# Kernel tuning notes

Hardware: AMD Instinct MI355X
Metric: run time of the kernel (lower is better)

Reference implementation:

```python
import jax, jax.numpy as jnp
import numpy as np

N, D, K = 4096, 1024, 32
MARGIN = 0.3
OP_TYPE = "weighty"


def setup_inputs() -> dict:
    key = jax.random.key(0)
    k1, k2, k3, k4, k5 = jax.random.split(key, 5)
    return {
        "inputs": jax.random.normal(k1, (N, D), jnp.float32),
        "prediction": jax.random.normal(k2, (N, K), jnp.float32),
        "targets": jax.random.randint(k3, (N,), 0, K),
        "true_targets": jax.random.randint(k4, (N,), 0, K),
        "prob": jax.random.uniform(k5, (N,), jnp.float32),
        "threshold": jnp.float32(0.5),
    }


def _weighty(d1, d2, pair_type, op_type):
    # vectorized translation of weighty_new
    if op_type == "mean":
        return (d1 + d2) / 2.0
    if op_type == "max":
        return jnp.maximum(d1, d2)
    if op_type == "min":
        return jnp.minimum(d1, d2)
    if op_type == "max-min":
        return jnp.maximum(d1, d2) if pair_type == 1 else jnp.minimum(d1, d2)
    # op_type == 'weighty'
    if pair_type == 1:
        e1, e2 = jnp.exp(d1), jnp.exp(d2)
        return (e1 * d1 + e2 * d2) / (e1 + e2)
    e1, e2 = jnp.exp(-d1), jnp.exp(-d2)
    return (e1 * d1 + e2 * d2) / (e1 + e2 + 1e-6)


def reference(inputs, prediction, targets, true_targets, prob, threshold):
    n = inputs.shape[0]
    rows = jnp.arange(n)
    # pairwise euclidean dist (GEMM-based, matches addmm_ formulation)
    sq = jnp.sum(inputs * inputs, axis=1)
    dist = sq[:, None] + sq[None, :] - 2.0 * (inputs @ inputs.T)
    dist = jnp.sqrt(jnp.clip(dist, 1e-12, None))  # [n, n]

    same = targets[:, None] == targets[None, :]
    conf = prob >= threshold

    # negatives sorted ascending by dist; positives sorted descending by dist
    neg_order = jnp.argsort(jnp.where(~same, dist, jnp.inf), axis=1)   # [n,n]
    pos_order = jnp.argsort(jnp.where(same, -dist, jnp.inf), axis=1)   # [n,n]
    hp = pos_order[:, 0]   # hardest positive (max dist)
    hn = neg_order[:, 0]   # hardest negative (min dist)
    d_ap = dist[rows, hp]
    d_an = dist[rows, hn]

    cp = prob[hp] >= threshold
    cn = prob[hn] >= threshold
    fn = jnp.argmax(prediction, axis=1)[hn] == targets  # hard neg is a false negative

    # neg re-selection: ranks 1..10 first with prob>=t, else rank 11 (loop_cnt cap 10)
    neg_cand = neg_order[:, 1:12]                       # [n,11]
    ok_n = prob[neg_cand] >= threshold
    sel_n = jnp.where(ok_n[:, :10].any(axis=1), jnp.argmax(ok_n[:, :10], axis=1), 10)
    d_nn = dist[rows, neg_cand[rows, sel_n]]

    # pos re-selection: descending ranks 1..5 first with prob>=t, else rank 6 (loop_cnt cap 5)
    pos_cand = pos_order[:, 1:7]                        # [n,6]
    ok_p = prob[pos_cand] >= threshold
    sel_p = jnp.where(ok_p[:, :5].any(axis=1), jnp.argmax(ok_p[:, :5], axis=1), 5)
    d_np = dist[rows, pos_cand[rows, sel_p]]

    w1 = _weighty(d_ap, d_an, 1, OP_TYPE)
    w0 = _weighty(d_ap, d_an, 0, OP_TYPE)

    case_b = cp & (~cn) & fn                 # confident pos, unconfident FN neg
    case_cd = (~cp) & (cn | (~fn))           # unconfident pos branches that re-select pos
    inv = (~cp) & (~cn) & fn                 # inverse loss branch

    ap = jnp.where(case_b, w1, jnp.where(case_cd, d_np, d_ap))
    an = jnp.where(case_b, d_nn, jnp.where(case_cd, w0, d_an))

    per = jnp.where(inv,
                    jax.nn.relu(an - ap + MARGIN),
                    jax.nn.relu(ap - an + MARGIN))
    conff = conf.astype(per.dtype)
    cnt = jnp.sum(conf.astype(jnp.int32))
    loss = jnp.where(cnt > 0, jnp.sum(per * conff) / jnp.maximum(cnt, 1).astype(per.dtype), 0.0)
    correct = jnp.sum(((an >= ap) & conf).astype(jnp.int32))
    return loss, correct, cnt
```

## Files before the change

kernel.cpp:

```cpp
#include <hip/hip_runtime.h>
#include <hip/hip_bf16.h>
#include <stdint.h>

typedef _Float16 half8 __attribute__((ext_vector_type(8)));
typedef _Float16 half4 __attribute__((ext_vector_type(4)));
typedef float f32x4 __attribute__((ext_vector_type(4)));
typedef unsigned long long u64;

#define N_ROWS 4096
#define DIM 1024
#define KCLS 32
#define MARGIN_F 0.3f
#define SENTN 0xFFFFFFFFFFFFFFFFull

typedef const __attribute__((address_space(1))) void GASV;
typedef __attribute__((address_space(3))) void LASV;

__device__ __forceinline__ void gload_lds16(const void* g, void* l) {
    __builtin_amdgcn_global_load_lds((GASV*)g, (LASV*)l, 16, 0, 0);
}

__global__ __launch_bounds__(256) void prep_kernel(
    const float* __restrict__ inputs, const float* __restrict__ prediction,
    _Float16* __restrict__ xh, float* __restrict__ sq, int* __restrict__ pred_cls)
{
    int wid = threadIdx.x >> 6, lane = threadIdx.x & 63;
    int r = blockIdx.x * 4 + wid;
    const float* row = inputs + (size_t)r * DIM;
    _Float16* hrow = xh + (size_t)r * DIM;
    float s = 0.f;
#pragma unroll
    for (int c = 0; c < 4; ++c) {
        int idx = lane * 4 + c * 256;
        float4 v = *(const float4*)(row + idx);
        s += v.x * v.x + v.y * v.y + v.z * v.z + v.w * v.w;
        half4 h;
        h.x = (_Float16)v.x; h.y = (_Float16)v.y;
        h.z = (_Float16)v.z; h.w = (_Float16)v.w;
        *(half4*)(hrow + idx) = h;
    }
#pragma unroll
    for (int off = 32; off; off >>= 1) s += __shfl_xor(s, off);

    u64 key = 0ull;
    if (lane < KCLS) {
        unsigned b = __float_as_uint(prediction[(size_t)r * KCLS + lane]);
        unsigned u = (b & 0x80000000u) ? ~b : (b | 0x80000000u);
        key = ((u64)u << 32) | (unsigned)(KCLS - 1 - lane);
    }
#pragma unroll
    for (int off = 32; off; off >>= 1) {
        u64 o = __shfl_xor(key, off);
        if (o > key) key = o;
    }
    if (lane == 0) {
        sq[r] = s;
        pred_cls[r] = KCLS - 1 - (int)(key & 0xFFFFFFFFu);
    }
}

__global__ __launch_bounds__(512) void gemm_kernel(
    const _Float16* __restrict__ X, const float* __restrict__ sq,
    float* __restrict__ out, int mode, int rb0)
{
    __shared__ __align__(16) _Float16 As[128 * 64];
    __shared__ __align__(16) _Float16 Bs[128 * 64];
    int tid = threadIdx.x;

    int bx, by;
    bool diag = false, mirror = false;
    if (mode == 0) {
        int u = ((int)blockIdx.x & 7) * 66 + ((int)blockIdx.x >> 3);
        int t_ = (int)((sqrtf(8.f * u + 1.f) - 1.f) * 0.5f);
        while ((t_ + 1) * (t_ + 2) / 2 <= u) ++t_;
        while (t_ * (t_ + 1) / 2 > u) --t_;
        by = t_;
        bx = u - t_ * (t_ + 1) / 2;
        diag = (bx == by);
        mirror = !diag;
    } else {
        int nwg = gridDim.x;
        int q = nwg >> 3;
        int swz = ((int)blockIdx.x & 7) * q + ((int)blockIdx.x >> 3);
        int nbx = nwg / 32;
        bx = swz % nbx;
        by = swz / nbx;
    }

    int rs = tid >> 3;
    int ss = tid & 7;
    int srcslot = ss ^ (rs & 7);
    const _Float16* gA = X + (size_t)(rb0 + bx * 128 + rs) * DIM + srcslot * 8;
    const _Float16* gB = X + (size_t)(by * 128 + rs) * DIM + srcslot * 8;
    _Float16* lA = As + tid * 8;
    _Float16* lB = Bs + tid * 8;

    int wid = tid >> 6, lane = tid & 63;
    int wr = (wid >> 2) * 64, wc = (wid & 3) * 32;
    int fr = lane & 15, q4 = lane >> 4;

    f32x4 acc[4][2];
#pragma unroll
    for (int m = 0; m < 4; ++m)
#pragma unroll
        for (int n = 0; n < 2; ++n) acc[m][n] = (f32x4){0.f, 0.f, 0.f, 0.f};

    for (int k0 = 0; k0 < DIM; k0 += 64) {
#pragma unroll
        for (int p = 0; p < 2; ++p) {
            gload_lds16(gA + k0 + (size_t)(p * 64) * DIM, lA + p * 4096);
            if (!diag) gload_lds16(gB + k0 + (size_t)(p * 64) * DIM, lB + p * 4096);
        }
        __syncthreads();
        const _Float16* Bsrc = diag ? As : Bs;
#pragma unroll
        for (int ks = 0; ks < 2; ++ks) {
            half8 a[4], b[2];
#pragma unroll
            for (int m = 0; m < 4; ++m) {
                int row = wr + m * 16 + fr;
                int s = (ks * 4 + q4) ^ (row & 7);
                a[m] = *(const half8*)(As + row * 64 + s * 8);
            }
#pragma unroll
            for (int n = 0; n < 2; ++n) {
                int brow = wc + n * 16 + fr;
                int s = (ks * 4 + q4) ^ (brow & 7);
                b[n] = *(const half8*)(Bsrc + brow * 64 + s * 8);
            }
#pragma unroll
            for (int m = 0; m < 4; ++m)
#pragma unroll
                for (int n = 0; n < 2; ++n)
                    acc[m][n] = __builtin_amdgcn_mfma_f32_16x16x32_f16(a[m], b[n], acc[m][n], 0, 0, 0);
        }
        __syncthreads();
    }

    int rbase = rb0 + bx * 128 + wr + q4 * 4;
    float sqr_[4][4];
#pragma unroll
    for (int m = 0; m < 4; ++m)
#pragma unroll
        for (int q = 0; q < 4; ++q) sqr_[m][q] = sq[rbase + m * 16 + q];

#pragma unroll
    for (int n = 0; n < 2; ++n) {
        int col = by * 128 + wc + n * 16 + fr;
        float sqc = sq[col];
#pragma unroll
        for (int m = 0; m < 4; ++m) {
            int row0 = rbase + m * 16;
            float4 d;
            d.x = fmaxf(sqr_[m][0] + sqc - 2.f * acc[m][n][0], 1e-12f);
            d.y = fmaxf(sqr_[m][1] + sqc - 2.f * acc[m][n][1], 1e-12f);
            d.z = fmaxf(sqr_[m][2] + sqc - 2.f * acc[m][n][2], 1e-12f);
            d.w = fmaxf(sqr_[m][3] + sqc - 2.f * acc[m][n][3], 1e-12f);
            out[(size_t)(row0 + 0) * N_ROWS + col] = d.x;
            out[(size_t)(row0 + 1) * N_ROWS + col] = d.y;
            out[(size_t)(row0 + 2) * N_ROWS + col] = d.z;
            out[(size_t)(row0 + 3) * N_ROWS + col] = d.w;
            if (mirror)
                *(float4*)&out[(size_t)col * N_ROWS + row0] = d;
        }
    }
}

__global__ __launch_bounds__(256) void select_kernel(
    const float* __restrict__ dot,
    const int* __restrict__ targets, const float* __restrict__ prob,
    const int* __restrict__ pred_cls, const float* __restrict__ thr_p,
    int rb0, float* __restrict__ per_term, int* __restrict__ corr_flag)
{
    __shared__ u64 Tn[4], Tp[4];
    __shared__ u64 negCand[64];
    __shared__ u64 posCand[64];
    __shared__ unsigned cnts[2];
    __shared__ u64 sN[12], sP[7];
    __shared__ u64 red[4];
    __shared__ u64 bcast;

    int t = threadIdx.x, lane = t & 63, w = t >> 6;
    int rloc = blockIdx.x, r = rb0 + rloc;
    int tr = targets[r];
    const float* drow = dot + (size_t)rloc * N_ROWS;

    if (t < 64) { negCand[t] = SENTN; posCand[t] = 0ull; }
    if (t < 2) cnts[t] = 0u;

    unsigned bits[16];
    unsigned maskSame = 0;
    u64 mneg = SENTN, mpos = 0ull;
#pragma unroll
    for (int q = 0; q < 4; ++q) {
        int col0 = q * 1024 + t * 4;
        float4 dv = *(const float4*)(drow + col0);
        int4 tv = *(const int4*)(targets + col0);
        int j = q * 4;
        unsigned b;
        b = __float_as_uint(dv.x); bits[j + 0] = b;
        if (tv.x == tr) { maskSame |= 1u << (j + 0);
            u64 pk = ((u64)b << 32) | (unsigned)(N_ROWS - 1 - (col0 + 0)); mpos = pk > mpos ? pk : mpos;
        } else { u64 nk = ((u64)b << 32) | (unsigned)(col0 + 0); mneg = nk < mneg ? nk : mneg; }
        b = __float_as_uint(dv.y); bits[j + 1] = b;
        if (tv.y == tr) { maskSame |= 1u << (j + 1);
            u64 pk = ((u64)b << 32) | (unsigned)(N_ROWS - 1 - (col0 + 1)); mpos = pk > mpos ? pk : mpos;
        } else { u64 nk = ((u64)b << 32) | (unsigned)(col0 + 1); mneg = nk < mneg ? nk : mneg; }
        b = __float_as_uint(dv.z); bits[j + 2] = b;
        if (tv.z == tr) { maskSame |= 1u << (j + 2);
            u64 pk = ((u64)b << 32) | (unsigned)(N_ROWS - 1 - (col0 + 2)); mpos = pk > mpos ? pk : mpos;
        } else { u64 nk = ((u64)b << 32) | (unsigned)(col0 + 2); mneg = nk < mneg ? nk : mneg; }
        b = __float_as_uint(dv.w); bits[j + 3] = b;
        if (tv.w == tr) { maskSame |= 1u << (j + 3);
            u64 pk = ((u64)b << 32) | (unsigned)(N_ROWS - 1 - (col0 + 3)); mpos = pk > mpos ? pk : mpos;
        } else { u64 nk = ((u64)b << 32) | (unsigned)(col0 + 3); mneg = nk < mneg ? nk : mneg; }
    }

    u64 T3 = SENTN, m = mneg;
#pragma unroll
    for (int rd = 0; rd < 3; ++rd) {
        u64 b = m;
#pragma unroll
        for (int off = 32; off; off >>= 1) {
            u64 o = __shfl_xor(b, off);
            b = o < b ? o : b;
        }
        T3 = b;
        if (m == b) m = SENTN;
    }
    u64 P2 = 0ull, mp = mpos;
#pragma unroll
    for (int rd = 0; rd < 2; ++rd) {
        u64 b = mp;
#pragma unroll
        for (int off = 32; off; off >>= 1) {
            u64 o = __shfl_xor(b, off);
            b = o > b ? o : b;
        }
        P2 = b;
        if (mp == b) mp = 0ull;
    }
    if (lane == 0) { Tn[w] = T3; Tp[w] = P2; }
    __syncthreads();

    u64 Tneg = Tn[0];
    Tneg = Tn[1] > Tneg ? Tn[1] : Tneg;
    Tneg = Tn[2] > Tneg ? Tn[2] : Tneg;
    Tneg = Tn[3] > Tneg ? Tn[3] : Tneg;
    u64 Tpos = Tp[0];
    Tpos = Tp[1] < Tpos ? Tp[1] : Tpos;
    Tpos = Tp[2] < Tpos ? Tp[2] : Tpos;
    Tpos = Tp[3] < Tpos ? Tp[3] : Tpos;
    unsigned TnB = (unsigned)(Tneg >> 32);
    unsigned TpB = (unsigned)(Tpos >> 32);

#pragma unroll
    for (int q = 0; q < 4; ++q) {
#pragma unroll
        for (int e = 0; e < 4; ++e) {
            int j = q * 4 + e;
            int col = q * 1024 + t * 4 + e;
            unsigned b = bits[j];
            bool same = (maskSame >> j) & 1u;
            if (!same && b <= TnB) {
                unsigned s = atomicAdd(&cnts[0], 1u);
                if (s < 64u) negCand[s] = ((u64)b << 32) | (unsigned)col;
            }
            if (same && b >= TpB) {
                unsigned s = atomicAdd(&cnts[1], 1u);
                if (s < 64u) posCand[s] = ((u64)b << 32) | (unsigned)(N_ROWS - 1 - col);
            }
        }
    }
    __syncthreads();

    bool fb = (cnts[0] > 64u) || (cnts[1] > 64u);

    if (!fb) {
        if (w == 0) {
            u64 v = negCand[lane];
#pragma unroll
            for (int k = 2; k <= 64; k <<= 1) {
#pragma unroll
                for (int j = 32; j; j >>= 1) {
                    if (j >= k) continue;
                    u64 o = __shfl_xor(v, j);
                    bool up = (lane & k) == 0;
                    bool small = (lane & j) == 0;
                    bool keepmin = (small == up);
                    u64 lo = v < o ? v : o, hi = v < o ? o : v;
                    v = keepmin ? lo : hi;
                }
            }
            if (lane < 12) sN[lane] = v;
        } else if (w == 1) {
            u64 v = ~posCand[lane];
#pragma unroll
            for (int k = 2; k <= 64; k <<= 1) {
#pragma unroll
                for (int j = 32; j; j >>= 1) {
                    if (j >= k) continue;
                    u64 o = __shfl_xor(v, j);
                    bool up = (lane & k) == 0;
                    bool small = (lane & j) == 0;
                    bool keepmin = (small == up);
                    u64 lo = v < o ? v : o, hi = v < o ? o : v;
                    v = keepmin ? lo : hi;
                }
            }
            if (lane < 7) sP[lane] = ~v;
        }
    } else {
        unsigned remN = 0, remP = 0;
        for (int rd = 0; rd < 12; ++rd) {
            u64 best = SENTN;
#pragma unroll
            for (int q = 0; q < 4; ++q)
#pragma unroll
                for (int e = 0; e < 4; ++e) {
                    int j = q * 4 + e;
                    int col = q * 1024 + t * 4 + e;
                    bool valid = !((maskSame >> j) & 1u) && !((remN >> j) & 1u);
                    u64 nk = valid ? (((u64)bits[j] << 32) | (unsigned)col) : SENTN;
                    best = nk < best ? nk : best;
                }
#pragma unroll
            for (int off = 32; off; off >>= 1) {
                u64 o = __shfl_xor(best, off);
                best = o < best ? o : best;
            }
            if (lane == 0) red[w] = best;
            __syncthreads();
            if (t == 0) {
                u64 b0 = red[0];
                b0 = red[1] < b0 ? red[1] : b0;
                b0 = red[2] < b0 ? red[2] : b0;
                b0 = red[3] < b0 ? red[3] : b0;
                sN[rd] = b0; bcast = b0;
            }
            __syncthreads();
            u64 b0 = bcast;
#pragma unroll
            for (int q = 0; q < 4; ++q)
#pragma unroll
                for (int e = 0; e < 4; ++e) {
                    int j = q * 4 + e;
                    int col = q * 1024 + t * 4 + e;
                    if ((((u64)bits[j] << 32) | (unsigned)col) == b0) remN |= 1u << j;
                }
            __syncthreads();
        }
        for (int rd = 0; rd < 7; ++rd) {
            u64 best = 0ull;
#pragma unroll
            for (int q = 0; q < 4; ++q)
#pragma unroll
                for (int e = 0; e < 4; ++e) {
                    int j = q * 4 + e;
                    int col = q * 1024 + t * 4 + e;
                    bool valid = ((maskSame >> j) & 1u) && !((remP >> j) & 1u);
                    u64 pk = valid ? (((u64)bits[j] << 32) | (unsigned)(N_ROWS - 1 - col)) : 0ull;
                    best = pk > best ? pk : best;
                }
#pragma unroll
            for (int off = 32; off; off >>= 1) {
                u64 o = __shfl_xor(best, off);
                best = o > best ? o : best;
            }
            if (lane == 0) red[w] = best;
            __syncthreads();
            if (t == 0) {
                u64 b0 = red[0];
                b0 = red[1] > b0 ? red[1] : b0;
                b0 = red[2] > b0 ? red[2] : b0;
                b0 = red[3] > b0 ? red[3] : b0;
                sP[rd] = b0; bcast = b0;
            }
            __syncthreads();
            u64 b0 = bcast;
#pragma unroll
            for (int q = 0; q < 4; ++q)
#pragma unroll
                for (int e = 0; e < 4; ++e) {
                    int j = q * 4 + e;
                    int col = q * 1024 + t * 4 + e;
                    if ((((u64)bits[j] << 32) | (unsigned)(N_ROWS - 1 - col)) == b0) remP |= 1u << j;
                }
            __syncthreads();
        }
    }
    __syncthreads();

    if (w == 0) {
        float thr = *thr_p;
        u64 kN = (lane < 12) ? sN[lane] : SENTN;
        u64 kP = (lane >= 32 && lane < 39) ? sP[lane - 32] : 0ull;
        int idxN = ((int)(kN & 0xFFFFFFFFull)) & (N_ROWS - 1);
        int idxP = (N_ROWS - 1 - (int)(kP & 0xFFFFFFFFull)) & (N_ROWS - 1);
        bool confN = (lane < 12) && kN != SENTN && (prob[idxN] >= thr);
        bool confP = (lane >= 32 && lane < 39) && kP != 0ull && (prob[idxP] >= thr);
        u64 balN = __ballot(confN);
        u64 balP = __ballot(confP);

        u64 mN_ = balN & 0x7FEull;
        int selN = mN_ ? (__ffsll(mN_) - 1) : 11;
        unsigned dnn_bits = __shfl((unsigned)(kN >> 32), selN);
        u64 mP_ = balP & (0x3Eull << 32);
        int selP = mP_ ? (__ffsll(mP_) - 1) : 38;
        unsigned dnp_bits = __shfl((unsigned)(kP >> 32), selP);
        unsigned dap_bits = __shfl((unsigned)(kP >> 32), 32);

        if (lane == 0) {
            float d_ap = sqrtf(__uint_as_float(dap_bits));
            float d_an = sqrtf(__uint_as_float((unsigned)(kN >> 32)));
            int hn = idxN;
            bool cp = (balP >> 32) & 1ull;
            bool cn = balN & 1ull;
            bool fn = (pred_cls[hn] == tr);
            float d_nn = sqrtf(__uint_as_float(dnn_bits));
            float d_np = sqrtf(__uint_as_float(dnp_bits));

            float e1p = __expf(d_ap), e2p = __expf(d_an);
            float w1 = (e1p * d_ap + e2p * d_an) / (e1p + e2p);
            float e1n = __expf(-d_ap), e2n = __expf(-d_an);
            float w0 = (e1n * d_ap + e2n * d_an) / (e1n + e2n + 1e-6f);
            bool case_b = cp && !cn && fn;
            bool case_cd = !cp && (cn || !fn);
            bool inv = !cp && !cn && fn;
            float ap = case_b ? w1 : (case_cd ? d_np : d_ap);
            float an = case_b ? d_nn : (case_cd ? w0 : d_an);
            float per = inv ? fmaxf(an - ap + MARGIN_F, 0.f)
                            : fmaxf(ap - an + MARGIN_F, 0.f);
            per_term[r] = per;
            corr_flag[r] = (an >= ap) ? 1 : 0;
        }
    }
}

__global__ __launch_bounds__(256) void finalize_kernel(
    const float* __restrict__ per_term, const int* __restrict__ corr_flag,
    const float* __restrict__ prob, const float* __restrict__ thr_p,
    float* __restrict__ out)
{
    __shared__ float sred[4]; __shared__ int cred[4]; __shared__ int nred[4];
    float thr = *thr_p;
    int t = threadIdx.x, lane = t & 63, wid = t >> 6;
    float s = 0.f; int c = 0, n = 0;
    for (int i = t; i < N_ROWS; i += 256) {
        if (prob[i] >= thr) {
            s += per_term[i];
            c += corr_flag[i];
            n += 1;
        }
    }
#pragma unroll
    for (int off = 32; off; off >>= 1) {
        s += __shfl_xor(s, off);
        c += __shfl_xor(c, off);
        n += __shfl_xor(n, off);
    }
    if (lane == 0) { sred[wid] = s; cred[wid] = c; nred[wid] = n; }
    __syncthreads();
    if (t == 0) {
        float ss = sred[0] + sred[1] + sred[2] + sred[3];
        int cc = cred[0] + cred[1] + cred[2] + cred[3];
        int nn = nred[0] + nred[1] + nred[2] + nred[3];
        float loss = (nn > 0) ? ss / (float)nn : 0.f;
        out[0] = loss;
        out[1] = (float)cc;
        out[2] = (float)nn;
    }
}

extern "C" void kernel_launch(void* const* d_in, const int* in_sizes, int n_in,
                              void* d_out, int out_size, void* d_ws, size_t ws_size,
                              hipStream_t stream)
{
    const float* inputs     = (const float*)d_in[0];
    const float* prediction = (const float*)d_in[1];
    const int*   targets    = (const int*)d_in[2];
    const float* prob       = (const float*)d_in[4];
    const float* thr        = (const float*)d_in[5];
    float* out = (float*)d_out;

    char* ws = (char*)d_ws;
    size_t off = 0;
    auto alloc = [&](size_t bytes) -> char* {
        char* p = ws + off;
        off = (off + bytes + 255) & ~(size_t)255;
        return p;
    };
    _Float16* xh     = (_Float16*)alloc((size_t)N_ROWS * DIM * sizeof(_Float16));
    float* sq        = (float*)alloc((size_t)N_ROWS * 4);
    int*   pred_cls  = (int*)alloc((size_t)N_ROWS * 4);
    float* per_term  = (float*)alloc((size_t)N_ROWS * 4);
    int*   corr_flag = (int*)alloc((size_t)N_ROWS * 4);

    size_t avail = (ws_size > off) ? (ws_size - off) : 0;
    size_t rowbytes = (size_t)N_ROWS * 4;
    int RB = 128;
    while (RB * 2 <= N_ROWS && (size_t)(RB * 2) * rowbytes <= avail) RB *= 2;
    float* dotbuf = (float*)alloc((size_t)RB * rowbytes);

    hipLaunchKernelGGL(prep_kernel, dim3(N_ROWS / 4), dim3(256), 0, stream,
                       inputs, prediction, xh, sq, pred_cls);
    if (RB == N_ROWS) {
        hipLaunchKernelGGL(gemm_kernel, dim3(528), dim3(512), 0, stream,
                           xh, sq, dotbuf, 0, 0);
        hipLaunchKernelGGL(select_kernel, dim3(N_ROWS), dim3(256), 0, stream,
                           dotbuf, targets, prob, pred_cls, thr, 0,
                           per_term, corr_flag);
    } else {
        for (int rb0 = 0; rb0 < N_ROWS; rb0 += RB) {
            hipLaunchKernelGGL(gemm_kernel, dim3((RB / 128) * 32), dim3(512), 0, stream,
                               xh, sq, dotbuf, 1, rb0);
            hipLaunchKernelGGL(select_kernel, dim3(RB), dim3(256), 0, stream,
                               dotbuf, targets, prob, pred_cls, thr, rb0,
                               per_term, corr_flag);
        }
    }
    hipLaunchKernelGGL(finalize_kernel, dim3(1), dim3(256), 0, stream,
                       per_term, corr_flag, prob, thr, out);
}
```

Before: 84.12 us.

## Pack same-class flag into distance LSB to drop target loads in select

The GEMM epilogue now loads row and column targets and stores the same-class flag in the least significant bit of each stored squared distance. The select kernel reads that bit instead of loading the targets array per column. This lets the first-pass min/max reductions run on 32-bit keys rather than 64-bit packed keys, which halves shuffle traffic. The cost is a one-ulp perturbation of the distances, which can change tie-breaking (the first pass no longer breaks ties by index) and slightly change the distance values.

```diff
diff --git a/kernel.cpp b/kernel.cpp
--- a/kernel.cpp
+++ b/kernel.cpp
@@ -61,6 +61,7 @@
 
 __global__ __launch_bounds__(512) void gemm_kernel(
     const _Float16* __restrict__ X, const float* __restrict__ sq,
+    const int* __restrict__ targets,
     float* __restrict__ out, int mode, int rb0)
 {
     __shared__ __align__(16) _Float16 As[128 * 64];
@@ -139,23 +140,33 @@
 
     int rbase = rb0 + bx * 128 + wr + q4 * 4;
     float sqr_[4][4];
+    int trr[4][4];
 #pragma unroll
     for (int m = 0; m < 4; ++m)
 #pragma unroll
-        for (int q = 0; q < 4; ++q) sqr_[m][q] = sq[rbase + m * 16 + q];
+        for (int q = 0; q < 4; ++q) {
+            sqr_[m][q] = sq[rbase + m * 16 + q];
+            trr[m][q] = targets[rbase + m * 16 + q];
+        }
 
 #pragma unroll
     for (int n = 0; n < 2; ++n) {
         int col = by * 128 + wc + n * 16 + fr;
         float sqc = sq[col];
+        int tc = targets[col];
 #pragma unroll
         for (int m = 0; m < 4; ++m) {
             int row0 = rbase + m * 16;
             float4 d;
-            d.x = fmaxf(sqr_[m][0] + sqc - 2.f * acc[m][n][0], 1e-12f);
-            d.y = fmaxf(sqr_[m][1] + sqc - 2.f * acc[m][n][1], 1e-12f);
-            d.z = fmaxf(sqr_[m][2] + sqc - 2.f * acc[m][n][2], 1e-12f);
-            d.w = fmaxf(sqr_[m][3] + sqc - 2.f * acc[m][n][3], 1e-12f);
+            unsigned u0, u1, u2, u3;
+            u0 = __float_as_uint(fmaxf(sqr_[m][0] + sqc - 2.f * acc[m][n][0], 1e-12f));
+            u1 = __float_as_uint(fmaxf(sqr_[m][1] + sqc - 2.f * acc[m][n][1], 1e-12f));
+            u2 = __float_as_uint(fmaxf(sqr_[m][2] + sqc - 2.f * acc[m][n][2], 1e-12f));
+            u3 = __float_as_uint(fmaxf(sqr_[m][3] + sqc - 2.f * acc[m][n][3], 1e-12f));
+            d.x = __uint_as_float((u0 & ~1u) | (unsigned)(trr[m][0] == tc));
+            d.y = __uint_as_float((u1 & ~1u) | (unsigned)(trr[m][1] == tc));
+            d.z = __uint_as_float((u2 & ~1u) | (unsigned)(trr[m][2] == tc));
+            d.w = __uint_as_float((u3 & ~1u) | (unsigned)(trr[m][3] == tc));
             out[(size_t)(row0 + 0) * N_ROWS + col] = d.x;
             out[(size_t)(row0 + 1) * N_ROWS + col] = d.y;
             out[(size_t)(row0 + 2) * N_ROWS + col] = d.z;
@@ -172,7 +183,7 @@
     const int* __restrict__ pred_cls, const float* __restrict__ thr_p,
     int rb0, float* __restrict__ per_term, int* __restrict__ corr_flag)
 {
-    __shared__ u64 Tn[4], Tp[4];
+    __shared__ unsigned Tn[4], Tp[4];
     __shared__ u64 negCand[64];
     __shared__ u64 posCand[64];
     __shared__ unsigned cnts[2];
@@ -182,77 +193,64 @@
 
     int t = threadIdx.x, lane = t & 63, w = t >> 6;
     int rloc = blockIdx.x, r = rb0 + rloc;
-    int tr = targets[r];
     const float* drow = dot + (size_t)rloc * N_ROWS;
 
     if (t < 64) { negCand[t] = SENTN; posCand[t] = 0ull; }
     if (t < 2) cnts[t] = 0u;
 
     unsigned bits[16];
-    unsigned maskSame = 0;
-    u64 mneg = SENTN, mpos = 0ull;
+    unsigned mneg = 0xFFFFFFFFu, mpos = 0u;
 #pragma unroll
     for (int q = 0; q < 4; ++q) {
         int col0 = q * 1024 + t * 4;
         float4 dv = *(const float4*)(drow + col0);
-        int4 tv = *(const int4*)(targets + col0);
         int j = q * 4;
         unsigned b;
         b = __float_as_uint(dv.x); bits[j + 0] = b;
-        if (tv.x == tr) { maskSame |= 1u << (j + 0);
-            u64 pk = ((u64)b << 32) | (unsigned)(N_ROWS - 1 - (col0 + 0)); mpos = pk > mpos ? pk : mpos;
-        } else { u64 nk = ((u64)b << 32) | (unsigned)(col0 + 0); mneg = nk < mneg ? nk : mneg; }
+        if (b & 1u) mpos = mpos > b ? mpos : b; else mneg = mneg < b ? mneg : b;
         b = __float_as_uint(dv.y); bits[j + 1] = b;
-        if (tv.y == tr) { maskSame |= 1u << (j + 1);
-            u64 pk = ((u64)b << 32) | (unsigned)(N_ROWS - 1 - (col0 + 1)); mpos = pk > mpos ? pk : mpos;
-        } else { u64 nk = ((u64)b << 32) | (unsigned)(col0 + 1); mneg = nk < mneg ? nk : mneg; }
+        if (b & 1u) mpos = mpos > b ? mpos : b; else mneg = mneg < b ? mneg : b;
         b = __float_as_uint(dv.z); bits[j + 2] = b;
-        if (tv.z == tr) { maskSame |= 1u << (j + 2);
-            u64 pk = ((u64)b << 32) | (unsigned)(N_ROWS - 1 - (col0 + 2)); mpos = pk > mpos ? pk : mpos;
-        } else { u64 nk = ((u64)b << 32) | (unsigned)(col0 + 2); mneg = nk < mneg ? nk : mneg; }
+        if (b & 1u) mpos = mpos > b ? mpos : b; else mneg = mneg < b ? mneg : b;
         b = __float_as_uint(dv.w); bits[j + 3] = b;
-        if (tv.w == tr) { maskSame |= 1u << (j + 3);
-            u64 pk = ((u64)b << 32) | (unsigned)(N_ROWS - 1 - (col0 + 3)); mpos = pk > mpos ? pk : mpos;
-        } else { u64 nk = ((u64)b << 32) | (unsigned)(col0 + 3); mneg = nk < mneg ? nk : mneg; }
-    }
-
-    u64 T3 = SENTN, m = mneg;
+        if (b & 1u) mpos = mpos > b ? mpos : b; else mneg = mneg < b ? mneg : b;
+    }
+
+    unsigned T3 = 0xFFFFFFFFu, m = mneg;
 #pragma unroll
     for (int rd = 0; rd < 3; ++rd) {
-        u64 b = m;
+        unsigned b = m;
 #pragma unroll
         for (int off = 32; off; off >>= 1) {
-            u64 o = __shfl_xor(b, off);
+            unsigned o = __shfl_xor(b, off);
             b = o < b ? o : b;
         }
         T3 = b;
-        if (m == b) m = SENTN;
-    }
-    u64 P2 = 0ull, mp = mpos;
+        if (m == b) m = 0xFFFFFFFFu;
+    }
+    unsigned P2 = 0u, mp = mpos;
 #pragma unroll
     for (int rd = 0; rd < 2; ++rd) {
-        u64 b = mp;
+        unsigned b = mp;
 #pragma unroll
         for (int off = 32; off; off >>= 1) {
-            u64 o = __shfl_xor(b, off);
+            unsigned o = __shfl_xor(b, off);
             b = o > b ? o : b;
         }
         P2 = b;
-        if (mp == b) mp = 0ull;
+        if (mp == b) mp = 0u;
     }
     if (lane == 0) { Tn[w] = T3; Tp[w] = P2; }
     __syncthreads();
 
-    u64 Tneg = Tn[0];
-    Tneg = Tn[1] > Tneg ? Tn[1] : Tneg;
-    Tneg = Tn[2] > Tneg ? Tn[2] : Tneg;
-    Tneg = Tn[3] > Tneg ? Tn[3] : Tneg;
-    u64 Tpos = Tp[0];
-    Tpos = Tp[1] < Tpos ? Tp[1] : Tpos;
-    Tpos = Tp[2] < Tpos ? Tp[2] : Tpos;
-    Tpos = Tp[3] < Tpos ? Tp[3] : Tpos;
-    unsigned TnB = (unsigned)(Tneg >> 32);
-    unsigned TpB = (unsigned)(Tpos >> 32);
+    unsigned TnB = Tn[0];
+    TnB = Tn[1] > TnB ? Tn[1] : TnB;
+    TnB = Tn[2] > TnB ? Tn[2] : TnB;
+    TnB = Tn[3] > TnB ? Tn[3] : TnB;
+    unsigned TpB = Tp[0];
+    TpB = Tp[1] < TpB ? Tp[1] : TpB;
+    TpB = Tp[2] < TpB ? Tp[2] : TpB;
+    TpB = Tp[3] < TpB ? Tp[3] : TpB;
 
 #pragma unroll
     for (int q = 0; q < 4; ++q) {
@@ -261,12 +259,11 @@
             int j = q * 4 + e;
             int col = q * 1024 + t * 4 + e;
             unsigned b = bits[j];
-            bool same = (maskSame >> j) & 1u;
-            if (!same && b <= TnB) {
+            if (!(b & 1u) && b <= TnB) {
                 unsigned s = atomicAdd(&cnts[0], 1u);
                 if (s < 64u) negCand[s] = ((u64)b << 32) | (unsigned)col;
             }
-            if (same && b >= TpB) {
+            if ((b & 1u) && b >= TpB) {
                 unsigned s = atomicAdd(&cnts[1], 1u);
                 if (s < 64u) posCand[s] = ((u64)b << 32) | (unsigned)(N_ROWS - 1 - col);
             }
@@ -320,7 +317,7 @@
                 for (int e = 0; e < 4; ++e) {
                     int j = q * 4 + e;
                     int col = q * 1024 + t * 4 + e;
-                    bool valid = !((maskSame >> j) & 1u) && !((remN >> j) & 1u);
+                    bool valid = !(bits[j] & 1u) && !((remN >> j) & 1u);
                     u64 nk = valid ? (((u64)bits[j] << 32) | (unsigned)col) : SENTN;
                     best = nk < best ? nk : best;
                 }
@@ -358,7 +355,7 @@
                 for (int e = 0; e < 4; ++e) {
                     int j = q * 4 + e;
                     int col = q * 1024 + t * 4 + e;
-                    bool valid = ((maskSame >> j) & 1u) && !((remP >> j) & 1u);
+                    bool valid = (bits[j] & 1u) && !((remP >> j) & 1u);
                     u64 pk = valid ? (((u64)bits[j] << 32) | (unsigned)(N_ROWS - 1 - col)) : 0ull;
                     best = pk > best ? pk : best;
                 }
@@ -393,6 +390,7 @@
 
     if (w == 0) {
         float thr = *thr_p;
+        int tr = targets[r];
         u64 kN = (lane < 12) ? sN[lane] : SENTN;
         u64 kP = (lane >= 32 && lane < 39) ? sP[lane - 32] : 0ull;
         int idxN = ((int)(kN & 0xFFFFFFFFull)) & (N_ROWS - 1);
@@ -506,14 +504,14 @@
                        inputs, prediction, xh, sq, pred_cls);
     if (RB == N_ROWS) {
         hipLaunchKernelGGL(gemm_kernel, dim3(528), dim3(512), 0, stream,
-                           xh, sq, dotbuf, 0, 0);
+                           xh, sq, targets, dotbuf, 0, 0);
         hipLaunchKernelGGL(select_kernel, dim3(N_ROWS), dim3(256), 0, stream,
                            dotbuf, targets, prob, pred_cls, thr, 0,
                            per_term, corr_flag);
     } else {
         for (int rb0 = 0; rb0 < N_ROWS; rb0 += RB) {
             hipLaunchKernelGGL(gemm_kernel, dim3((RB / 128) * 32), dim3(512), 0, stream,
-                               xh, sq, dotbuf, 1, rb0);
+                               xh, sq, targets, dotbuf, 1, rb0);
             hipLaunchKernelGGL(select_kernel, dim3(RB), dim3(256), 0, stream,
                                dotbuf, targets, prob, pred_cls, thr, rb0,
                                per_term, corr_flag);
```

Measured after the change: 83.53 us. About the same (-0.7%).
